# Optimization experiments

Measured on AMD Instinct MI355X. Metric: run time of the kernel, lower is better.

The kernel has to match this reference:

```python
import jax, jax.numpy as jnp
import numpy as np

D_IN = 2048
H1 = D_IN // 4      # 512
H2 = D_IN // 16     # 128
N_EXP = 8
N_CLS = 10
BATCH = 16384


def setup_inputs() -> dict:
    key = jax.random.key(0)
    ks = jax.random.split(key, 16)
    s = lambda k, shape, fan_in: jax.random.normal(k, shape, jnp.float32) / np.sqrt(fan_in)
    return {
        "fs": jax.random.normal(ks[0], (BATCH, D_IN // 2), jnp.float32),
        "fp": jax.random.normal(ks[1], (BATCH, D_IN // 2), jnp.float32),
        # gate MLP params (output = num_source, softmax)
        "gW1": s(ks[2], (D_IN, H1), D_IN), "gb1": jnp.zeros((H1,), jnp.float32),
        "gW2": s(ks[3], (H1, H2), H1),     "gb2": jnp.zeros((H2,), jnp.float32),
        "gW3": s(ks[4], (H2, N_EXP), H2), "gb3": jnp.zeros((N_EXP,), jnp.float32),
        # stacked expert MLP params (output = num classes, log_softmax)
        "eW1": s(ks[5], (N_EXP, D_IN, H1), D_IN), "eb1": jnp.zeros((N_EXP, H1), jnp.float32),
        "eW2": s(ks[6], (N_EXP, H1, H2), H1),     "eb2": jnp.zeros((N_EXP, H2), jnp.float32),
        "eW3": s(ks[7], (N_EXP, H2, N_CLS), H2),  "eb3": jnp.zeros((N_EXP, N_CLS), jnp.float32),
    }


def reference(fs, fp, gW1, gb1, gW2, gb2, gW3, gb3, eW1, eb1, eW2, eb2, eW3, eb3):
    features = jnp.concatenate([fs, fp], axis=-1)            # [B, D_IN]

    # Gate MLP on detached features (detach is a no-op for fwd), softmax output
    g = jax.nn.relu(features @ gW1 + gb1)
    g = jax.nn.relu(g @ gW2 + gb2)
    gate_outs = jax.nn.softmax(g @ gW3 + gb3, axis=-1)       # [B, E]

    # All experts as batched GEMMs over stacked weights, log_softmax output
    h = jax.nn.relu(jnp.einsum('bd,edh->beh', features, eW1) + eb1[None])   # [B, E, H1]
    h = jax.nn.relu(jnp.einsum('beh,ehk->bek', h, eW2) + eb2[None])         # [B, E, H2]
    logits = jnp.einsum('bek,eko->beo', h, eW3) + eb3[None]                 # [B, E, C]
    expert_outs = jax.nn.log_softmax(logits, axis=-1)                       # [B, E, C]

    # Gate-weighted sum over experts
    output = jnp.einsum('be,bec->bc', gate_outs, expert_outs)               # [B, C]
    return output, gate_outs
```

## Files before the change

### kernel.cpp

```cpp
#include <hip/hip_runtime.h>
#include <hip/hip_bf16.h>

#define B_SZ   16384
#define DIN    2048
#define H1_SZ  512
#define H2_SZ  128
#define N_EXP  8
#define N_CLS  10
#define N1     4608
#define N2     1152

typedef __attribute__((ext_vector_type(8))) __bf16 bf16x8;
typedef __attribute__((ext_vector_type(4))) float  floatx4;
typedef __attribute__((ext_vector_type(4))) short  short4v;
typedef __attribute__((ext_vector_type(8))) short  short8v;

__device__ __forceinline__ float bf2f(short s) {
  unsigned int u = ((unsigned int)(unsigned short)s) << 16;
  float f; __builtin_memcpy(&f, &u, 4); return f;
}

__global__ void convert_features_kernel(const float* __restrict__ fs,
                                        const float* __restrict__ fp,
                                        __hip_bfloat16* __restrict__ X) {
  const int nf4 = B_SZ * (DIN / 4);
  const float4* fs4 = (const float4*)fs;
  const float4* fp4 = (const float4*)fp;
  for (int i = blockIdx.x * blockDim.x + threadIdx.x; i < nf4;
       i += gridDim.x * blockDim.x) {
    int c = i & 511;
    int row = i >> 9;
    float4 v = (c < 256) ? fs4[(size_t)row * 256 + c]
                         : fp4[(size_t)row * 256 + (c - 256)];
    union { short4v v4; __hip_bfloat16 h[4]; } u;
    u.h[0] = __float2bfloat16(v.x);
    u.h[1] = __float2bfloat16(v.y);
    u.h[2] = __float2bfloat16(v.z);
    u.h[3] = __float2bfloat16(v.w);
    *(short4v*)(X + (size_t)i * 4) = u.v4;
  }
}

__global__ void transpose_convert_kernel(const float* __restrict__ expert_src,
                                         const float* __restrict__ gate_src,
                                         int K, int H, int E,
                                         __hip_bfloat16* __restrict__ out) {
  __shared__ float t[32][33];
  int k0 = blockIdx.x * 32;
  int n0 = blockIdx.y * 32;
  int e = n0 / H;
  const float* src; int h0;
  if (e < E) { src = expert_src + (size_t)e * K * H; h0 = n0 - e * H; }
  else       { src = gate_src;                       h0 = n0 - E * H; }
  int tx = threadIdx.x, ty = threadIdx.y;
  #pragma unroll
  for (int j = 0; j < 4; ++j) {
    int r = ty + j * 8;
    t[r][tx] = src[(size_t)(k0 + r) * H + h0 + tx];
  }
  __syncthreads();
  #pragma unroll
  for (int j = 0; j < 4; ++j) {
    int r = ty + j * 8;
    out[(size_t)(n0 + r) * K + k0 + tx] = __float2bfloat16(t[tx][r]);
  }
}

__device__ __forceinline__ void gemm_core(
    const __hip_bfloat16* __restrict__ A,  int lda,
    const __hip_bfloat16* __restrict__ BT, int K,
    const float* __restrict__ bias,
    __hip_bfloat16* __restrict__ O, int ldo) {
  __shared__ __align__(16) __hip_bfloat16 As[128 * 64];
  __shared__ __align__(16) __hip_bfloat16 Bs[128 * 64];

  const int tid  = threadIdx.x;
  const int lane = tid & 63;
  const int wave = tid >> 6;
  const int wm   = (wave >> 1) * 64;
  const int wn   = (wave & 1) * 64;
  const int lrow  = lane & 15;
  const int lquad = lane >> 4;

  floatx4 acc[4][4] = {};

  for (int k0 = 0; k0 < K; k0 += 64) {
    #pragma unroll
    for (int j = 0; j < 4; ++j) {
      int chunk = j * 256 + tid;
      int mi = chunk >> 3;
      int cs = chunk & 7;
      int cl = cs ^ (mi & 7);
      __builtin_amdgcn_global_load_lds(
          (const __attribute__((address_space(1))) unsigned int*)(A + (size_t)mi * lda + k0 + cl * 8),
          (__attribute__((address_space(3))) unsigned int*)(As + chunk * 8),
          16, 0, 0);
      __builtin_amdgcn_global_load_lds(
          (const __attribute__((address_space(1))) unsigned int*)(BT + (size_t)mi * K + k0 + cl * 8),
          (__attribute__((address_space(3))) unsigned int*)(Bs + chunk * 8),
          16, 0, 0);
    }
    __syncthreads();
    #pragma unroll
    for (int ks = 0; ks < 2; ++ks) {
      bf16x8 a[4], b[4];
      #pragma unroll
      for (int t = 0; t < 4; ++t) {
        int ar = wm + t * 16 + lrow;
        int br = wn + t * 16 + lrow;
        int ca = (ks * 4 + lquad) ^ (ar & 7);
        int cb = (ks * 4 + lquad) ^ (br & 7);
        a[t] = *(const bf16x8*)(As + ar * 64 + ca * 8);
        b[t] = *(const bf16x8*)(Bs + br * 64 + cb * 8);
      }
      #pragma unroll
      for (int mt = 0; mt < 4; ++mt)
        #pragma unroll
        for (int nt = 0; nt < 4; ++nt)
          acc[mt][nt] = __builtin_amdgcn_mfma_f32_16x16x32_bf16(
              a[mt], b[nt], acc[mt][nt], 0, 0, 0);
    }
    __syncthreads();
  }

  #pragma unroll
  for (int nt = 0; nt < 4; ++nt) {
    int col = wn + nt * 16 + lrow;
    float bv = bias[col];
    #pragma unroll
    for (int mt = 0; mt < 4; ++mt) {
      #pragma unroll
      for (int r = 0; r < 4; ++r) {
        int row = wm + mt * 16 + lquad * 4 + r;
        float v = acc[mt][nt][r] + bv;
        v = v > 0.f ? v : 0.f;
        O[(size_t)row * ldo + col] = __float2bfloat16(v);
      }
    }
  }
}

__global__ __launch_bounds__(256, 2) void gemm1_kernel(
    const __hip_bfloat16* __restrict__ X, const __hip_bfloat16* __restrict__ W1T,
    const float* __restrict__ eb1, const float* __restrict__ gb1,
    __hip_bfloat16* __restrict__ H1) {
  int m0 = blockIdx.y * 128;
  int n0 = blockIdx.x * 128;
  const float* bias = (n0 < N_EXP * H1_SZ) ? (eb1 + n0) : (gb1 + (n0 - N_EXP * H1_SZ));
  gemm_core(X + (size_t)m0 * DIN, DIN,
            W1T + (size_t)n0 * DIN, DIN,
            bias,
            H1 + (size_t)m0 * N1 + n0, N1);
}

__global__ __launch_bounds__(256, 2) void gemm2_kernel(
    const __hip_bfloat16* __restrict__ H1, const __hip_bfloat16* __restrict__ W2T,
    const float* __restrict__ eb2, const float* __restrict__ gb2,
    __hip_bfloat16* __restrict__ H2) {
  int m0 = blockIdx.y * 128;
  int z  = blockIdx.z;
  const float* bias = (z < N_EXP) ? (eb2 + z * H2_SZ) : gb2;
  gemm_core(H1 + (size_t)m0 * N1 + z * H1_SZ, N1,
            W2T + (size_t)z * H2_SZ * H1_SZ, H1_SZ,
            bias,
            H2 + (size_t)m0 * N2 + z * H2_SZ, N2);
}

__global__ __launch_bounds__(256) void layer3_kernel(
    const __hip_bfloat16* __restrict__ H2,
    const float* __restrict__ gW3, const float* __restrict__ gb3,
    const float* __restrict__ eW3, const float* __restrict__ eb3,
    float* __restrict__ out, float* __restrict__ gate_out) {
  int tid  = threadIdx.x;
  int j    = tid & 7;
  int rloc = tid >> 3;
  long row = (long)blockIdx.x * 32 + rloc;
  const __hip_bfloat16* hrow = H2 + row * N2;

  float accg = 0.f;
  float acc[N_CLS];
  #pragma unroll
  for (int c = 0; c < N_CLS; ++c) acc[c] = 0.f;

  #pragma unroll 4
  for (int k8 = 0; k8 < 16; ++k8) {
    short8v hg8 = *(const short8v*)(hrow + N_EXP * H2_SZ + k8 * 8);
    short8v he8 = *(const short8v*)(hrow + j * H2_SZ + k8 * 8);
    #pragma unroll
    for (int t = 0; t < 8; ++t) {
      int k = k8 * 8 + t;
      float hg = bf2f(hg8[t]);
      float he = bf2f(he8[t]);
      accg += hg * gW3[k * N_EXP + j];
      const float* w = eW3 + (size_t)(j * H2_SZ + k) * N_CLS;
      #pragma unroll
      for (int c = 0; c < N_CLS; ++c) acc[c] += he * w[c];
    }
  }

  float gj = accg + gb3[j];
  float mx = gj;
  mx = fmaxf(mx, __shfl_xor(mx, 1));
  mx = fmaxf(mx, __shfl_xor(mx, 2));
  mx = fmaxf(mx, __shfl_xor(mx, 4));
  float ex = __expf(gj - mx);
  float s = ex;
  s += __shfl_xor(s, 1);
  s += __shfl_xor(s, 2);
  s += __shfl_xor(s, 4);
  float gp = ex / s;

  float lg[N_CLS];
  float lm = -1e30f;
  #pragma unroll
  for (int c = 0; c < N_CLS; ++c) {
    lg[c] = acc[c] + eb3[j * N_CLS + c];
    lm = fmaxf(lm, lg[c]);
  }
  float es = 0.f;
  #pragma unroll
  for (int c = 0; c < N_CLS; ++c) es += __expf(lg[c] - lm);
  float lse = lm + __logf(es);

  float o[N_CLS];
  #pragma unroll
  for (int c = 0; c < N_CLS; ++c) o[c] = gp * (lg[c] - lse);
  #pragma unroll
  for (int c = 0; c < N_CLS; ++c) {
    o[c] += __shfl_xor(o[c], 1);
    o[c] += __shfl_xor(o[c], 2);
    o[c] += __shfl_xor(o[c], 4);
  }

  gate_out[row * N_EXP + j] = gp;
  if (j == 0) {
    #pragma unroll
    for (int c = 0; c < N_CLS; ++c) out[row * N_CLS + c] = o[c];
  }
}

extern "C" void kernel_launch(void* const* d_in, const int* in_sizes, int n_in,
                              void* d_out, int out_size, void* d_ws, size_t ws_size,
                              hipStream_t stream) {
  const float* fs  = (const float*)d_in[0];
  const float* fp  = (const float*)d_in[1];
  const float* gW1 = (const float*)d_in[2];
  const float* gb1 = (const float*)d_in[3];
  const float* gW2 = (const float*)d_in[4];
  const float* gb2 = (const float*)d_in[5];
  const float* gW3 = (const float*)d_in[6];
  const float* gb3 = (const float*)d_in[7];
  const float* eW1 = (const float*)d_in[8];
  const float* eb1 = (const float*)d_in[9];
  const float* eW2 = (const float*)d_in[10];
  const float* eb2 = (const float*)d_in[11];
  const float* eW3 = (const float*)d_in[12];
  const float* eb3 = (const float*)d_in[13];
  float* out = (float*)d_out;

  char* ws = (char*)d_ws;
  __hip_bfloat16* X   = (__hip_bfloat16*)ws;
  __hip_bfloat16* H2  = X;
  __hip_bfloat16* W1T = (__hip_bfloat16*)(ws + 67108864);
  __hip_bfloat16* W2T = (__hip_bfloat16*)(ws + 85983232);
  __hip_bfloat16* H1  = (__hip_bfloat16*)(ws + 87162880);

  convert_features_kernel<<<2048, 256, 0, stream>>>(fs, fp, X);
  transpose_convert_kernel<<<dim3(DIN / 32, N1 / 32), dim3(32, 8), 0, stream>>>(
      eW1, gW1, DIN, H1_SZ, N_EXP, W1T);
  transpose_convert_kernel<<<dim3(H1_SZ / 32, N2 / 32), dim3(32, 8), 0, stream>>>(
      eW2, gW2, H1_SZ, H2_SZ, N_EXP, W2T);
  gemm1_kernel<<<dim3(N1 / 128, B_SZ / 128), 256, 0, stream>>>(X, W1T, eb1, gb1, H1);
  gemm2_kernel<<<dim3(1, B_SZ / 128, N_EXP + 1), 256, 0, stream>>>(H1, W2T, eb2, gb2, H2);
  layer3_kernel<<<B_SZ / 32, 256, 0, stream>>>(H2, gW3, gb3, eW3, eb3,
                                               out, out + (size_t)B_SZ * N_CLS);
}
```

Before: 602.3 us.

## Fuse layer-1 and layer-2 GEMMs per expert, keeping hidden activations in LDS

Replaces the separate gemm1 and gemm2 kernels with one kernel. Each block computes a 64-row by 512-column layer-1 tile for one expert (or the gate), applies bias and ReLU, and stores the result swizzled in LDS. It then runs the layer-2 GEMM straight from LDS and writes only the H2 output. This removes the large bf16 H1 round trip through global memory and one launch. In exchange the block needs 80 KB of dynamic LDS and uses a narrower M tile, which may lower occupancy and change GEMM efficiency.

New measurement: 631.8 us. 1.05x slower.

```diff
diff --git a/kernel.cpp b/kernel.cpp
--- a/kernel.cpp
+++ b/kernel.cpp
@@ -66,38 +66,52 @@
   }
 }
 
-__device__ __forceinline__ void gemm_core(
-    const __hip_bfloat16* __restrict__ A,  int lda,
-    const __hip_bfloat16* __restrict__ BT, int K,
-    const float* __restrict__ bias,
-    __hip_bfloat16* __restrict__ O, int ldo) {
-  __shared__ __align__(16) __hip_bfloat16 As[128 * 64];
-  __shared__ __align__(16) __hip_bfloat16 Bs[128 * 64];
+__global__ __launch_bounds__(512, 4) void fused12_kernel(
+    const __hip_bfloat16* __restrict__ X,
+    const __hip_bfloat16* __restrict__ W1T,
+    const __hip_bfloat16* __restrict__ W2T,
+    const float* __restrict__ eb1, const float* __restrict__ gb1,
+    const float* __restrict__ eb2, const float* __restrict__ gb2,
+    __hip_bfloat16* __restrict__ H2) {
+  extern __shared__ __align__(16) __hip_bfloat16 smem[];
+  __hip_bfloat16* As  = smem;
+  __hip_bfloat16* Bs  = smem + 4096;
+  __hip_bfloat16* C1L = smem;
+  __hip_bfloat16* Bs2 = smem + 32768;
 
   const int tid  = threadIdx.x;
   const int lane = tid & 63;
   const int wave = tid >> 6;
-  const int wm   = (wave >> 1) * 64;
-  const int wn   = (wave & 1) * 64;
   const int lrow  = lane & 15;
   const int lquad = lane >> 4;
 
+  const int z  = blockIdx.x;
+  const int m0 = blockIdx.y * 64;
+
+  const __hip_bfloat16* Ab = X   + (size_t)m0 * DIN;
+  const __hip_bfloat16* Bb = W1T + (size_t)z * H1_SZ * DIN;
+  const __hip_bfloat16* W2b = W2T + (size_t)z * H2_SZ * H1_SZ;
+  const float* bias1 = (z < N_EXP) ? (eb1 + z * H1_SZ) : gb1;
+  const float* bias2 = (z < N_EXP) ? (eb2 + z * H2_SZ) : gb2;
+
+  const int wn = wave * 64;
   floatx4 acc[4][4] = {};
 
-  for (int k0 = 0; k0 < K; k0 += 64) {
-    #pragma unroll
-    for (int j = 0; j < 4; ++j) {
-      int chunk = j * 256 + tid;
-      int mi = chunk >> 3;
-      int cs = chunk & 7;
-      int cl = cs ^ (mi & 7);
+  for (int k0 = 0; k0 < DIN; k0 += 64) {
+    {
+      int mi = tid >> 3, cs = tid & 7, cl = cs ^ (mi & 7);
       __builtin_amdgcn_global_load_lds(
-          (const __attribute__((address_space(1))) unsigned int*)(A + (size_t)mi * lda + k0 + cl * 8),
-          (__attribute__((address_space(3))) unsigned int*)(As + chunk * 8),
+          (const __attribute__((address_space(1))) unsigned int*)(Ab + (size_t)mi * DIN + k0 + cl * 8),
+          (__attribute__((address_space(3))) unsigned int*)(As + tid * 8),
           16, 0, 0);
+    }
+    #pragma unroll
+    for (int j = 0; j < 8; ++j) {
+      int idx = j * 512 + tid;
+      int row = idx >> 3, cs = idx & 7, cl = cs ^ (row & 7);
       __builtin_amdgcn_global_load_lds(
-          (const __attribute__((address_space(1))) unsigned int*)(BT + (size_t)mi * K + k0 + cl * 8),
-          (__attribute__((address_space(3))) unsigned int*)(Bs + chunk * 8),
+          (const __attribute__((address_space(1))) unsigned int*)(Bb + (size_t)row * DIN + k0 + cl * 8),
+          (__attribute__((address_space(3))) unsigned int*)(Bs + idx * 8),
           16, 0, 0);
     }
     __syncthreads();
@@ -106,7 +120,7 @@
       bf16x8 a[4], b[4];
       #pragma unroll
       for (int t = 0; t < 4; ++t) {
-        int ar = wm + t * 16 + lrow;
+        int ar = t * 16 + lrow;
         int br = wn + t * 16 + lrow;
         int ca = (ks * 4 + lquad) ^ (ar & 7);
         int cb = (ks * 4 + lquad) ^ (br & 7);
@@ -126,44 +140,72 @@
   #pragma unroll
   for (int nt = 0; nt < 4; ++nt) {
     int col = wn + nt * 16 + lrow;
-    float bv = bias[col];
+    float bv = bias1[col];
     #pragma unroll
     for (int mt = 0; mt < 4; ++mt) {
       #pragma unroll
       for (int r = 0; r < 4; ++r) {
-        int row = wm + mt * 16 + lquad * 4 + r;
+        int row = mt * 16 + lquad * 4 + r;
         float v = acc[mt][nt][r] + bv;
         v = v > 0.f ? v : 0.f;
-        O[(size_t)row * ldo + col] = __float2bfloat16(v);
+        int cc = (((col >> 3) ^ (row & 7)) << 3) | (col & 7);
+        C1L[row * 512 + cc] = __float2bfloat16(v);
       }
     }
   }
-}
-
-__global__ __launch_bounds__(256, 2) void gemm1_kernel(
-    const __hip_bfloat16* __restrict__ X, const __hip_bfloat16* __restrict__ W1T,
-    const float* __restrict__ eb1, const float* __restrict__ gb1,
-    __hip_bfloat16* __restrict__ H1) {
-  int m0 = blockIdx.y * 128;
-  int n0 = blockIdx.x * 128;
-  const float* bias = (n0 < N_EXP * H1_SZ) ? (eb1 + n0) : (gb1 + (n0 - N_EXP * H1_SZ));
-  gemm_core(X + (size_t)m0 * DIN, DIN,
-            W1T + (size_t)n0 * DIN, DIN,
-            bias,
-            H1 + (size_t)m0 * N1 + n0, N1);
-}
-
-__global__ __launch_bounds__(256, 2) void gemm2_kernel(
-    const __hip_bfloat16* __restrict__ H1, const __hip_bfloat16* __restrict__ W2T,
-    const float* __restrict__ eb2, const float* __restrict__ gb2,
-    __hip_bfloat16* __restrict__ H2) {
-  int m0 = blockIdx.y * 128;
-  int z  = blockIdx.z;
-  const float* bias = (z < N_EXP) ? (eb2 + z * H2_SZ) : gb2;
-  gemm_core(H1 + (size_t)m0 * N1 + z * H1_SZ, N1,
-            W2T + (size_t)z * H2_SZ * H1_SZ, H1_SZ,
-            bias,
-            H2 + (size_t)m0 * N2 + z * H2_SZ, N2);
+
+  const int wm2 = (wave >> 2) * 32;
+  const int wn2 = (wave & 3) * 32;
+  floatx4 acc2[2][2] = {};
+
+  for (int k0 = 0; k0 < H1_SZ; k0 += 64) {
+    #pragma unroll
+    for (int j = 0; j < 2; ++j) {
+      int idx = j * 512 + tid;
+      int row = idx >> 3, cs = idx & 7, cl = cs ^ (row & 7);
+      __builtin_amdgcn_global_load_lds(
+          (const __attribute__((address_space(1))) unsigned int*)(W2b + (size_t)row * H1_SZ + k0 + cl * 8),
+          (__attribute__((address_space(3))) unsigned int*)(Bs2 + idx * 8),
+          16, 0, 0);
+    }
+    __syncthreads();
+    #pragma unroll
+    for (int ks = 0; ks < 2; ++ks) {
+      bf16x8 a2[2], b2[2];
+      #pragma unroll
+      for (int t = 0; t < 2; ++t) {
+        int ar = wm2 + t * 16 + lrow;
+        int kch = (k0 >> 3) + ks * 4 + lquad;
+        a2[t] = *(const bf16x8*)(C1L + ar * 512 + ((kch ^ (ar & 7)) << 3));
+        int br = wn2 + t * 16 + lrow;
+        int cb = (ks * 4 + lquad) ^ (br & 7);
+        b2[t] = *(const bf16x8*)(Bs2 + br * 64 + cb * 8);
+      }
+      #pragma unroll
+      for (int mt = 0; mt < 2; ++mt)
+        #pragma unroll
+        for (int nt = 0; nt < 2; ++nt)
+          acc2[mt][nt] = __builtin_amdgcn_mfma_f32_16x16x32_bf16(
+              a2[mt], b2[nt], acc2[mt][nt], 0, 0, 0);
+    }
+    __syncthreads();
+  }
+
+  #pragma unroll
+  for (int nt = 0; nt < 2; ++nt) {
+    int col = wn2 + nt * 16 + lrow;
+    float bv = bias2[col];
+    #pragma unroll
+    for (int mt = 0; mt < 2; ++mt) {
+      #pragma unroll
+      for (int r = 0; r < 4; ++r) {
+        int row = wm2 + mt * 16 + lquad * 4 + r;
+        float v = acc2[mt][nt][r] + bv;
+        v = v > 0.f ? v : 0.f;
+        H2[(size_t)(m0 + row) * N2 + z * H2_SZ + col] = __float2bfloat16(v);
+      }
+    }
+  }
 }
 
 __global__ __launch_bounds__(256) void layer3_kernel(
@@ -260,18 +302,17 @@
 
   char* ws = (char*)d_ws;
   __hip_bfloat16* X   = (__hip_bfloat16*)ws;
-  __hip_bfloat16* H2  = X;
   __hip_bfloat16* W1T = (__hip_bfloat16*)(ws + 67108864);
   __hip_bfloat16* W2T = (__hip_bfloat16*)(ws + 85983232);
-  __hip_bfloat16* H1  = (__hip_bfloat16*)(ws + 87162880);
+  __hip_bfloat16* H2  = (__hip_bfloat16*)(ws + 87162880);
 
   convert_features_kernel<<<2048, 256, 0, stream>>>(fs, fp, X);
   transpose_convert_kernel<<<dim3(DIN / 32, N1 / 32), dim3(32, 8), 0, stream>>>(
       eW1, gW1, DIN, H1_SZ, N_EXP, W1T);
   transpose_convert_kernel<<<dim3(H1_SZ / 32, N2 / 32), dim3(32, 8), 0, stream>>>(
       eW2, gW2, H1_SZ, H2_SZ, N_EXP, W2T);
-  gemm1_kernel<<<dim3(N1 / 128, B_SZ / 128), 256, 0, stream>>>(X, W1T, eb1, gb1, H1);
-  gemm2_kernel<<<dim3(1, B_SZ / 128, N_EXP + 1), 256, 0, stream>>>(H1, W2T, eb2, gb2, H2);
+  fused12_kernel<<<dim3(N_EXP + 1, B_SZ / 64), 512, 81920, stream>>>(
+      X, W1T, W2T, eb1, gb1, eb2, gb2, H2);
   layer3_kernel<<<B_SZ / 32, 256, 0, stream>>>(H2, gW3, gb3, eW3, eb3,
                                                out, out + (size_t)B_SZ * N_CLS);
 }
```
